# Performance work log

Measured on AMD Instinct MI355X. Metric: run time of the kernel, lower is better.

## Reference

```python
import jax, jax.numpy as jnp
import numpy as np

B, C_IN, N = 64, 64, 4097          # N = T + 1 (index 0 is the null node)
T = N - 1
HID, LAT = 128, 64
EPS = 1e-5


def _tree_conv(trees, children, W, b):
    # trees: (B, C, N); children: (B, 3T) int indices into node axis
    Bn, C, _ = trees.shape
    idx = jnp.broadcast_to(children[:, None, :], (Bn, C, children.shape[1]))
    g = jnp.take_along_axis(trees, idx, axis=2)        # (B, C, 3T) gather
    g = g.reshape(Bn, C, -1, 3)                        # (B, C, T, 3)
    out = jnp.einsum('bctk,ock->bot', g, W) + b[None, :, None]  # (B, O, T)
    zero = jnp.zeros((Bn, out.shape[1], 1), out.dtype)  # null-node column
    return jnp.concatenate([zero, out], axis=2)         # (B, O, T+1)


def _tree_layer_norm(x):
    # normalize over (channels, nodes) per example; torch.std -> ddof=1
    mean = jnp.mean(x, axis=(1, 2), keepdims=True)
    std = jnp.std(x, axis=(1, 2), ddof=1, keepdims=True)
    return (x - mean) / (std + EPS)


def _encode(feats, children, W1, b1, W2, b2):
    x = _tree_conv(feats, children, W1, b1)
    x = jax.nn.relu(_tree_layer_norm(x))
    x = _tree_conv(x, children, W2, b2)
    x = jax.nn.relu(_tree_layer_norm(x))   # dropout is identity in eval
    return jnp.max(x, axis=2)              # DynamicPooling: (B, HID)


def setup_inputs() -> dict:
    key = jax.random.key(0)
    ks = jax.random.split(key, 12)
    s_in = 1.0 / np.sqrt(3 * C_IN)
    s_h = 1.0 / np.sqrt(3 * HID)
    s_fc = 1.0 / np.sqrt(2 * HID)
    return {
        'logical_feats': jax.random.normal(ks[0], (B, C_IN, N), jnp.float32),
        'physical_feats': jax.random.normal(ks[1], (B, C_IN, N), jnp.float32),
        'children': jax.random.randint(ks[2], (B, 3 * T), 0, N, jnp.int32),
        'Wl1': jax.random.normal(ks[3], (HID, C_IN, 3), jnp.float32) * s_in,
        'bl1': jnp.zeros((HID,), jnp.float32),
        'Wl2': jax.random.normal(ks[4], (HID, HID, 3), jnp.float32) * s_h,
        'bl2': jnp.zeros((HID,), jnp.float32),
        'Wp1': jax.random.normal(ks[5], (HID, C_IN, 3), jnp.float32) * s_in,
        'bp1': jnp.zeros((HID,), jnp.float32),
        'Wp2': jax.random.normal(ks[6], (HID, HID, 3), jnp.float32) * s_h,
        'bp2': jnp.zeros((HID,), jnp.float32),
        'Wmu': jax.random.normal(ks[7], (LAT, 2 * HID), jnp.float32) * s_fc,
        'bmu': jnp.zeros((LAT,), jnp.float32),
        'Wlv': jax.random.normal(ks[8], (LAT, 2 * HID), jnp.float32) * s_fc,
        'blv': jnp.zeros((LAT,), jnp.float32),
    }


def reference(logical_feats, physical_feats, children,
              Wl1, bl1, Wl2, bl2, Wp1, bp1, Wp2, bp2,
              Wmu, bmu, Wlv, blv):
    # NOTE: source module passes log_children to BOTH encoders; kept faithful.
    l_embed = _encode(logical_feats, children, Wl1, bl1, Wl2, bl2)
    p_embed = _encode(physical_feats, children, Wp1, bp1, Wp2, bp2)
    combined = jnp.concatenate([l_embed, p_embed], axis=-1)  # (B, 2*HID)
    mu = combined @ Wmu.T + bmu
    logvar = combined @ Wlv.T + blv
    return mu, logvar
```

## Files before the change

kernel.cpp:

```cpp
#include <hip/hip_runtime.h>
#include <hip/hip_bf16.h>

#define NODES 4097
#define TT 4096
#define CIN 64
#define HID 128
#define BATCH 64
#define EPS 1e-5f

typedef short bf16x8 __attribute__((ext_vector_type(8)));
typedef float f32x16 __attribute__((ext_vector_type(16)));

__device__ __forceinline__ void load_lds16(const void* g, void* l) {
    __builtin_amdgcn_global_load_lds(
        (const __attribute__((address_space(1))) unsigned int*)(uintptr_t)g,
        (__attribute__((address_space(3))) unsigned int*)(uintptr_t)l,
        16, 0, 0);
}

__global__ __launch_bounds__(256) void k_transpose(const float* __restrict__ f0,
                                                   const float* __restrict__ f1,
                                                   __hip_bfloat16* __restrict__ out) {
    __shared__ float tile[32][33];
    int z = blockIdx.z;
    int enc = z >> 6, b = z & 63;
    const float* in = enc ? f1 : f0;
    __hip_bfloat16* o = out + (size_t)enc * BATCH * NODES * CIN;
    int n0 = blockIdx.x * 32;
    int c0 = blockIdx.y * 32;
    int tx = threadIdx.x, ty = threadIdx.y;
    for (int i = 0; i < 32; i += 8) {
        int n = n0 + tx, c = c0 + ty + i;
        float v = 0.f;
        if (n < NODES) v = in[((size_t)b * CIN + c) * NODES + n];
        tile[ty + i][tx] = v;
    }
    __syncthreads();
    for (int i = 0; i < 32; i += 8) {
        int n = n0 + ty + i, c = c0 + tx;
        if (n < NODES) o[((size_t)b * NODES + n) * CIN + c] = __float2bfloat16(tile[tx][ty + i]);
    }
}

__global__ void k_wprep(const float* __restrict__ W0, const float* __restrict__ W1,
                        __hip_bfloat16* __restrict__ Wp, int C) {
    int enc = blockIdx.y;
    const float* W = enc ? W1 : W0;
    __hip_bfloat16* o = Wp + (size_t)enc * 3 * C * HID;
    int id = blockIdx.x * 256 + threadIdx.x;
    int total = 3 * C * HID / 8;
    if (id >= total) return;
    int lane = id & 63;
    int ct = (id >> 6) & 3;
    int ks = id >> 8;
    int n = ct * 32 + (lane & 31);
    int kb = ks * 16 + (lane >> 5) * 8;
    union { int4 i; __hip_bfloat16 h[8]; } u;
#pragma unroll
    for (int j = 0; j < 8; ++j) {
        int k = kb + j;
        int slot = k / C, c = k % C;
        u.h[j] = __float2bfloat16(W[(n * C + c) * 3 + slot]);
    }
    ((int4*)o)[id] = u.i;
}

template <int C, int NPH, bool POOL>
__global__ __launch_bounds__(256) void k_conv_mfma(
    const __hip_bfloat16* __restrict__ xT,
    const int* __restrict__ children,
    const __hip_bfloat16* __restrict__ Wp,
    const float* __restrict__ bias0, const float* __restrict__ bias1,
    __hip_bfloat16* __restrict__ y,
    float* __restrict__ sums,
    float* __restrict__ pool_part) {
    constexpr int KSc = C / 16;
    constexpr int TOTK = 3 * KSc;
    constexpr int PK = TOTK / NPH;
    int L = blockIdx.x;
    int xcd = L & 7;
    int idx = L >> 3;
    int xt = idx & 63;
    int bg = (idx >> 6) & 7;
    int enc = idx >> 9;
    int b = xcd + 8 * bg;
    const int t0 = xt * 64;
    const int tid = threadIdx.x;
    const int lane = tid & 63;
    const int w = tid >> 6;
    const int rg2 = w >> 1, ct2 = w & 1;

    __shared__ __align__(16) char A_lds[2 * PK * 1024];

    const __hip_bfloat16* x = xT + (size_t)enc * BATCH * NODES * C;
    const int4* WpB = (const int4*)(Wp + (size_t)enc * 3 * C * HID);
    const float* bias = enc ? bias1 : bias0;
    const int sb = enc * BATCH + b;

    const size_t rowbase = (size_t)b * NODES;
    const long cb3 = (long)b * (3 * TT);
    const int tnode = t0 + rg2 * 32 + (lane & 31);

    const char* rowp[3];
#pragma unroll
    for (int s = 0; s < 3; ++s) {
        int child = children[cb3 + (long)tnode * 3 + s];
        rowp[s] = (const char*)(x + (rowbase + child) * C) + (lane >> 5) * 16;
    }

    f32x16 acc[2] = {};

#pragma unroll
    for (int ph = 0; ph < NPH; ++ph) {
        if (ph) __syncthreads();
#pragma unroll
        for (int i = 0; i < PK / 2; ++i) {
            int kk = (w & 1) * (PK / 2) + i;
            int ksg = ph * PK + kk;
            int slot = ksg / KSc, ksl = ksg % KSc;
            load_lds16(rowp[slot] + ksl * 32, A_lds + (rg2 * PK + kk) * 1024);
        }
        __syncthreads();
#pragma unroll
        for (int kk = 0; kk < PK; ++kk) {
            int ksg = ph * PK + kk;
            bf16x8 a = *(const bf16x8*)(A_lds + (rg2 * PK + kk) * 1024 + lane * 16);
            union { int4 i; bf16x8 v; } b0, b1;
            b0.i = WpB[(ksg * 4 + 2 * ct2 + 0) * 64 + lane];
            b1.i = WpB[(ksg * 4 + 2 * ct2 + 1) * 64 + lane];
            acc[0] = __builtin_amdgcn_mfma_f32_32x32x16_bf16(a, b0.v, acc[0], 0, 0, 0);
            acc[1] = __builtin_amdgcn_mfma_f32_32x32x16_bf16(a, b1.v, acc[1], 0, 0, 0);
        }
    }

    float bsum = 0.f, bss = 0.f;
    float lmax[2] = {-3.4e38f, -3.4e38f};
    __hip_bfloat16* yp = POOL ? nullptr : (y + (size_t)enc * BATCH * NODES * HID);
#pragma unroll
    for (int cti = 0; cti < 2; ++cti) {
        int o = 64 * ct2 + 32 * cti + (lane & 31);
        float bv = bias[o];
        int rbase = t0 + 32 * rg2 + 4 * (lane >> 5) + 1;
        f32x16 a = acc[cti];
#pragma unroll
        for (int reg = 0; reg < 16; ++reg) {
            float v = a[reg] + bv;
            bsum += v;
            bss += v * v;
            if (POOL) {
                lmax[cti] = fmaxf(lmax[cti], v);
            } else {
                int row = rbase + (reg & 3) + 8 * (reg >> 2);
                yp[(rowbase + row) * HID + o] = __float2bfloat16(v);
            }
        }
    }
    if (!POOL && xt == 0 && tid < HID)
        yp[rowbase * HID + tid] = __float2bfloat16(0.f);

    __syncthreads();
    float* red = (float*)A_lds;
    float* pm = red + 512;
    red[tid] = bsum;
    red[256 + tid] = bss;
    if (POOL) {
        int slice = 2 * rg2 + (lane >> 5);
        pm[(64 * ct2 + (lane & 31)) * 4 + slice] = lmax[0];
        pm[(64 * ct2 + 32 + (lane & 31)) * 4 + slice] = lmax[1];
    }
    __syncthreads();
    for (int s2 = 128; s2 > 0; s2 >>= 1) {
        if (tid < s2) { red[tid] += red[tid + s2]; red[256 + tid] += red[256 + tid + s2]; }
        __syncthreads();
    }
    if (tid == 0) {
        atomicAdd(&sums[sb * 2], red[0]);
        atomicAdd(&sums[sb * 2 + 1], red[256]);
    }
    if (POOL && tid < HID) {
        float m = fmaxf(fmaxf(pm[tid * 4], pm[tid * 4 + 1]),
                        fmaxf(pm[tid * 4 + 2], pm[tid * 4 + 3]));
        pool_part[((size_t)sb * 64 + xt) * HID + tid] = m;
    }
}

__global__ void k_stats(const float* __restrict__ sums, float* __restrict__ ms) {
    int s = threadIdx.x;
    const float M = (float)HID * (float)NODES;
    float S = sums[s * 2], SS = sums[s * 2 + 1];
    float mean = S / M;
    float var = (SS - S * S / M) / (M - 1.f);
    float sd = sqrtf(fmaxf(var, 0.f));
    ms[s * 2] = mean;
    ms[s * 2 + 1] = 1.f / (sd + EPS);
}

__global__ __launch_bounds__(256) void k_norm(__hip_bfloat16* __restrict__ y,
                                              const float* __restrict__ ms) {
    constexpr int Q = NODES * HID / 8;
    int s = blockIdx.y;
    int q = blockIdx.x * 256 + threadIdx.x;
    if (q >= Q) return;
    float mean = ms[s * 2], scale = ms[s * 2 + 1];
    int4* p = (int4*)(y + (size_t)s * NODES * HID) + q;
    union { int4 i; __hip_bfloat16 h[8]; } u;
    u.i = *p;
#pragma unroll
    for (int j = 0; j < 8; ++j) {
        float f = (__bfloat162float(u.h[j]) - mean) * scale;
        u.h[j] = __float2bfloat16(f > 0.f ? f : 0.f);
    }
    *p = u.i;
}

__global__ __launch_bounds__(128) void k_pool_fin(const float* __restrict__ part,
                                                  const float* __restrict__ ms1,
                                                  float* __restrict__ combined) {
    int b = blockIdx.x, enc = blockIdx.y, o = threadIdx.x;
    int sb = enc * BATCH + b;
    float m = 0.f;
#pragma unroll 4
    for (int s = 0; s < 64; ++s)
        m = fmaxf(m, part[((size_t)sb * 64 + s) * HID + o]);
    float v = (m - ms1[sb * 2]) * ms1[sb * 2 + 1];
    combined[b * 256 + enc * 128 + o] = v > 0.f ? v : 0.f;
}

__global__ __launch_bounds__(128) void k_fc(const float* __restrict__ combined,
                                            const float* __restrict__ Wmu, const float* __restrict__ bmu,
                                            const float* __restrict__ Wlv, const float* __restrict__ blv,
                                            float* __restrict__ out) {
    int b = blockIdx.x;
    int tid = threadIdx.x;
    __shared__ float cb[256];
    cb[tid] = combined[b * 256 + tid];
    cb[tid + 128] = combined[b * 256 + tid + 128];
    __syncthreads();
    const float* W = (tid < 64) ? Wmu : Wlv;
    int l = tid & 63;
    float s = (tid < 64) ? bmu[l] : blv[l];
    for (int j = 0; j < 256; ++j) s += cb[j] * W[l * 256 + j];
    out[(tid < 64 ? 0 : BATCH * 64) + b * 64 + l] = s;
}

extern "C" void kernel_launch(void* const* d_in, const int* in_sizes, int n_in,
                              void* d_out, int out_size, void* d_ws, size_t ws_size,
                              hipStream_t stream) {
    const int* children = (const int*)d_in[2];
    const float* Wmu = (const float*)d_in[11];
    const float* bmu = (const float*)d_in[12];
    const float* Wlv = (const float*)d_in[13];
    const float* blv = (const float*)d_in[14];

    char* ws = (char*)d_ws;
    size_t off = 0;
    auto alloc = [&](size_t bytes) { void* p = ws + off; off += (bytes + 255) & ~(size_t)255; return p; };
    float* sums = (float*)alloc(2 * 2 * BATCH * 2 * sizeof(float));
    float* msbuf = (float*)alloc(2 * 2 * BATCH * 2 * sizeof(float));
    float* combined = (float*)alloc((size_t)BATCH * 256 * sizeof(float));
    float* pool_part = (float*)alloc((size_t)2 * BATCH * 64 * HID * sizeof(float));
    __hip_bfloat16* Wp1 = (__hip_bfloat16*)alloc((size_t)2 * 3 * CIN * HID * sizeof(__hip_bfloat16));
    __hip_bfloat16* Wp2 = (__hip_bfloat16*)alloc((size_t)2 * 3 * HID * HID * sizeof(__hip_bfloat16));
    __hip_bfloat16* fT = (__hip_bfloat16*)alloc((size_t)2 * BATCH * NODES * CIN * sizeof(__hip_bfloat16));
    __hip_bfloat16* y1 = (__hip_bfloat16*)alloc((size_t)2 * BATCH * NODES * HID * sizeof(__hip_bfloat16));

    hipMemsetAsync(sums, 0, 2 * 2 * BATCH * 2 * sizeof(float), stream);

    k_wprep<<<dim3(3 * CIN * HID / 8 / 256, 2), 256, 0, stream>>>(
        (const float*)d_in[3], (const float*)d_in[7], Wp1, CIN);
    k_wprep<<<dim3(3 * HID * HID / 8 / 256, 2), 256, 0, stream>>>(
        (const float*)d_in[5], (const float*)d_in[9], Wp2, HID);
    k_transpose<<<dim3(129, 2, 2 * BATCH), dim3(32, 8), 0, stream>>>(
        (const float*)d_in[0], (const float*)d_in[1], fT);

    k_conv_mfma<CIN, 2, false><<<8192, 256, 0, stream>>>(
        fT, children, Wp1, (const float*)d_in[4], (const float*)d_in[8], y1, sums, nullptr);
    k_stats<<<1, 128, 0, stream>>>(sums, msbuf);
    k_norm<<<dim3((NODES * HID / 8 + 255) / 256, 2 * BATCH), 256, 0, stream>>>(y1, msbuf);
    k_conv_mfma<HID, 3, true><<<8192, 256, 0, stream>>>(
        y1, children, Wp2, (const float*)d_in[6], (const float*)d_in[10], nullptr,
        sums + 256, pool_part);
    k_stats<<<1, 128, 0, stream>>>(sums + 256, msbuf + 256);
    k_pool_fin<<<dim3(BATCH, 2), 128, 0, stream>>>(pool_part, msbuf + 256, combined);

    k_fc<<<BATCH, 128, 0, stream>>>(combined, Wmu, bmu, Wlv, blv, (float*)d_out);
}
```

Baseline: 486.1 us.

## Load gathered rows directly into registers and give each wave all 128 outputs

The conv kernel drops the LDS staging of gathered child rows via global_load_lds along with its phase barriers. Each wave now reads its A fragments straight from global memory into registers and computes all four 32-wide output tiles, so one A load feeds four MFMAs. Blocks now cover 128 nodes, which halves the grid and the number of pooling partials. In exchange each wave holds four accumulators (more VGPRs, possibly lower occupancy), the gathered loads are no longer coalesced through LDS, and B-fragment traffic per wave doubles.

```diff
diff --git a/kernel.cpp b/kernel.cpp
--- a/kernel.cpp
+++ b/kernel.cpp
@@ -10,13 +10,6 @@
 
 typedef short bf16x8 __attribute__((ext_vector_type(8)));
 typedef float f32x16 __attribute__((ext_vector_type(16)));
-
-__device__ __forceinline__ void load_lds16(const void* g, void* l) {
-    __builtin_amdgcn_global_load_lds(
-        (const __attribute__((address_space(1))) unsigned int*)(uintptr_t)g,
-        (__attribute__((address_space(3))) unsigned int*)(uintptr_t)l,
-        16, 0, 0);
-}
 
 __global__ __launch_bounds__(256) void k_transpose(const float* __restrict__ f0,
                                                    const float* __restrict__ f1,
@@ -65,7 +58,7 @@
     ((int4*)o)[id] = u.i;
 }
 
-template <int C, int NPH, bool POOL>
+template <int C, bool POOL>
 __global__ __launch_bounds__(256) void k_conv_mfma(
     const __hip_bfloat16* __restrict__ xT,
     const int* __restrict__ children,
@@ -75,99 +68,79 @@
     float* __restrict__ sums,
     float* __restrict__ pool_part) {
     constexpr int KSc = C / 16;
-    constexpr int TOTK = 3 * KSc;
-    constexpr int PK = TOTK / NPH;
+    constexpr int KS = 3 * KSc;
     int L = blockIdx.x;
     int xcd = L & 7;
     int idx = L >> 3;
-    int xt = idx & 63;
-    int bg = (idx >> 6) & 7;
-    int enc = idx >> 9;
+    int xt = idx & 31;
+    int bg = (idx >> 5) & 7;
+    int enc = idx >> 8;
     int b = xcd + 8 * bg;
-    const int t0 = xt * 64;
+    const int t0 = xt * 128;
     const int tid = threadIdx.x;
     const int lane = tid & 63;
     const int w = tid >> 6;
-    const int rg2 = w >> 1, ct2 = w & 1;
-
-    __shared__ __align__(16) char A_lds[2 * PK * 1024];
+    const int hi = lane >> 5;
 
     const __hip_bfloat16* x = xT + (size_t)enc * BATCH * NODES * C;
     const int4* WpB = (const int4*)(Wp + (size_t)enc * 3 * C * HID);
     const float* bias = enc ? bias1 : bias0;
     const int sb = enc * BATCH + b;
-
     const size_t rowbase = (size_t)b * NODES;
     const long cb3 = (long)b * (3 * TT);
-    const int tnode = t0 + rg2 * 32 + (lane & 31);
-
-    const char* rowp[3];
+    const int tnode = t0 + w * 32 + (lane & 31);
+
+    const int4* ap[3];
 #pragma unroll
     for (int s = 0; s < 3; ++s) {
         int child = children[cb3 + (long)tnode * 3 + s];
-        rowp[s] = (const char*)(x + (rowbase + child) * C) + (lane >> 5) * 16;
-    }
-
-    f32x16 acc[2] = {};
-
-#pragma unroll
-    for (int ph = 0; ph < NPH; ++ph) {
-        if (ph) __syncthreads();
-#pragma unroll
-        for (int i = 0; i < PK / 2; ++i) {
-            int kk = (w & 1) * (PK / 2) + i;
-            int ksg = ph * PK + kk;
-            int slot = ksg / KSc, ksl = ksg % KSc;
-            load_lds16(rowp[slot] + ksl * 32, A_lds + (rg2 * PK + kk) * 1024);
+        ap[s] = (const int4*)(x + (rowbase + child) * C) + hi;
+    }
+
+    f32x16 acc[4] = {};
+#pragma unroll
+    for (int ksg = 0; ksg < KS; ++ksg) {
+        int slot = ksg / KSc, ksl = ksg % KSc;
+        union { int4 i; bf16x8 v; } a;
+        a.i = ap[slot][ksl * 2];
+#pragma unroll
+        for (int cti = 0; cti < 4; ++cti) {
+            union { int4 i; bf16x8 v; } bb;
+            bb.i = WpB[(ksg * 4 + cti) * 64 + lane];
+            acc[cti] = __builtin_amdgcn_mfma_f32_32x32x16_bf16(a.v, bb.v, acc[cti], 0, 0, 0);
         }
-        __syncthreads();
-#pragma unroll
-        for (int kk = 0; kk < PK; ++kk) {
-            int ksg = ph * PK + kk;
-            bf16x8 a = *(const bf16x8*)(A_lds + (rg2 * PK + kk) * 1024 + lane * 16);
-            union { int4 i; bf16x8 v; } b0, b1;
-            b0.i = WpB[(ksg * 4 + 2 * ct2 + 0) * 64 + lane];
-            b1.i = WpB[(ksg * 4 + 2 * ct2 + 1) * 64 + lane];
-            acc[0] = __builtin_amdgcn_mfma_f32_32x32x16_bf16(a, b0.v, acc[0], 0, 0, 0);
-            acc[1] = __builtin_amdgcn_mfma_f32_32x32x16_bf16(a, b1.v, acc[1], 0, 0, 0);
-        }
-    }
-
+    }
+
+    __shared__ float red[512];
+    __shared__ float pm[1024];
     float bsum = 0.f, bss = 0.f;
-    float lmax[2] = {-3.4e38f, -3.4e38f};
     __hip_bfloat16* yp = POOL ? nullptr : (y + (size_t)enc * BATCH * NODES * HID);
-#pragma unroll
-    for (int cti = 0; cti < 2; ++cti) {
-        int o = 64 * ct2 + 32 * cti + (lane & 31);
+    const int rbase = t0 + w * 32 + 4 * hi + 1;
+#pragma unroll
+    for (int cti = 0; cti < 4; ++cti) {
+        int o = cti * 32 + (lane & 31);
         float bv = bias[o];
-        int rbase = t0 + 32 * rg2 + 4 * (lane >> 5) + 1;
         f32x16 a = acc[cti];
+        float lmax = -3.4e38f;
 #pragma unroll
         for (int reg = 0; reg < 16; ++reg) {
             float v = a[reg] + bv;
             bsum += v;
             bss += v * v;
             if (POOL) {
-                lmax[cti] = fmaxf(lmax[cti], v);
+                lmax = fmaxf(lmax, v);
             } else {
                 int row = rbase + (reg & 3) + 8 * (reg >> 2);
                 yp[(rowbase + row) * HID + o] = __float2bfloat16(v);
             }
         }
+        if (POOL) pm[o * 8 + w * 2 + hi] = lmax;
     }
     if (!POOL && xt == 0 && tid < HID)
         yp[rowbase * HID + tid] = __float2bfloat16(0.f);
 
-    __syncthreads();
-    float* red = (float*)A_lds;
-    float* pm = red + 512;
     red[tid] = bsum;
     red[256 + tid] = bss;
-    if (POOL) {
-        int slice = 2 * rg2 + (lane >> 5);
-        pm[(64 * ct2 + (lane & 31)) * 4 + slice] = lmax[0];
-        pm[(64 * ct2 + 32 + (lane & 31)) * 4 + slice] = lmax[1];
-    }
     __syncthreads();
     for (int s2 = 128; s2 > 0; s2 >>= 1) {
         if (tid < s2) { red[tid] += red[tid + s2]; red[256 + tid] += red[256 + tid + s2]; }
@@ -178,9 +151,10 @@
         atomicAdd(&sums[sb * 2 + 1], red[256]);
     }
     if (POOL && tid < HID) {
-        float m = fmaxf(fmaxf(pm[tid * 4], pm[tid * 4 + 1]),
-                        fmaxf(pm[tid * 4 + 2], pm[tid * 4 + 3]));
-        pool_part[((size_t)sb * 64 + xt) * HID + tid] = m;
+        float m = -3.4e38f;
+#pragma unroll
+        for (int s2 = 0; s2 < 8; ++s2) m = fmaxf(m, pm[tid * 8 + s2]);
+        pool_part[((size_t)sb * 32 + xt) * HID + tid] = m;
     }
 }
 
@@ -220,8 +194,8 @@
     int sb = enc * BATCH + b;
     float m = 0.f;
 #pragma unroll 4
-    for (int s = 0; s < 64; ++s)
-        m = fmaxf(m, part[((size_t)sb * 64 + s) * HID + o]);
+    for (int s = 0; s < 32; ++s)
+        m = fmaxf(m, part[((size_t)sb * 32 + s) * HID + o]);
     float v = (m - ms1[sb * 2]) * ms1[sb * 2 + 1];
     combined[b * 256 + enc * 128 + o] = v > 0.f ? v : 0.f;
 }
@@ -258,7 +232,7 @@
     float* sums = (float*)alloc(2 * 2 * BATCH * 2 * sizeof(float));
     float* msbuf = (float*)alloc(2 * 2 * BATCH * 2 * sizeof(float));
     float* combined = (float*)alloc((size_t)BATCH * 256 * sizeof(float));
-    float* pool_part = (float*)alloc((size_t)2 * BATCH * 64 * HID * sizeof(float));
+    float* pool_part = (float*)alloc((size_t)2 * BATCH * 32 * HID * sizeof(float));
     __hip_bfloat16* Wp1 = (__hip_bfloat16*)alloc((size_t)2 * 3 * CIN * HID * sizeof(__hip_bfloat16));
     __hip_bfloat16* Wp2 = (__hip_bfloat16*)alloc((size_t)2 * 3 * HID * HID * sizeof(__hip_bfloat16));
     __hip_bfloat16* fT = (__hip_bfloat16*)alloc((size_t)2 * BATCH * NODES * CIN * sizeof(__hip_bfloat16));
@@ -273,11 +247,11 @@
     k_transpose<<<dim3(129, 2, 2 * BATCH), dim3(32, 8), 0, stream>>>(
         (const float*)d_in[0], (const float*)d_in[1], fT);
 
-    k_conv_mfma<CIN, 2, false><<<8192, 256, 0, stream>>>(
+    k_conv_mfma<CIN, false><<<4096, 256, 0, stream>>>(
         fT, children, Wp1, (const float*)d_in[4], (const float*)d_in[8], y1, sums, nullptr);
     k_stats<<<1, 128, 0, stream>>>(sums, msbuf);
     k_norm<<<dim3((NODES * HID / 8 + 255) / 256, 2 * BATCH), 256, 0, stream>>>(y1, msbuf);
-    k_conv_mfma<HID, 3, true><<<8192, 256, 0, stream>>>(
+    k_conv_mfma<HID, true><<<4096, 256, 0, stream>>>(
         y1, children, Wp2, (const float*)d_in[6], (const float*)d_in[10], nullptr,
         sums + 256, pool_part);
     k_stats<<<1, 128, 0, stream>>>(sums + 256, msbuf + 256);
```

New measurement: 462.1 us. 4.9% less time.
